# Kernel tuning notes

Measured on AMD Instinct MI355X. Metric: run time of the kernel, lower is better.

## Reference

```python
import jax, jax.numpy as jnp
import numpy as np

DIM = 1536
HEADS = 12
HEAD_DIM = DIM // HEADS
EPS = 1e-6
IMG_LEN = 257


def _rmsnorm(x, g):
    var = jnp.mean(jnp.square(x), axis=-1, keepdims=True)
    return x * jax.lax.rsqrt(var + EPS) * g


def _attn(q, k, v):
    # q: [b, Lq, h, d], k/v: [b, Lk, h, d]
    scale = 1.0 / jnp.sqrt(jnp.asarray(HEAD_DIM, q.dtype))
    s = jnp.einsum('bqhd,bkhd->bhqk', q, k) * scale
    p = jax.nn.softmax(s, axis=-1)
    return jnp.einsum('bhqk,bkhd->bqhd', p, v)


def setup_inputs() -> dict:
    key = jax.random.key(0)
    ks = jax.random.split(key, 20)
    w = lambda k: jax.random.normal(k, (DIM, DIM), dtype=jnp.float32) * 0.02
    b = lambda k: jax.random.normal(k, (DIM,), dtype=jnp.float32) * 0.01
    return {
        'x': jax.random.normal(ks[0], (1, 16384, DIM), dtype=jnp.float32),
        'context': jax.random.normal(ks[1], (1, 769, DIM), dtype=jnp.float32),
        'context_lens': jax.random.randint(ks[2], (1,), 0, 512, dtype=jnp.int32),
        'Wq': w(ks[3]), 'bq': b(ks[4]),
        'Wk': w(ks[5]), 'bk': b(ks[6]),
        'Wv': w(ks[7]), 'bv': b(ks[8]),
        'W_addk': w(ks[9]), 'b_addk': b(ks[10]),
        'W_addv': w(ks[11]), 'b_addv': b(ks[12]),
        'Wo': w(ks[13]), 'bo': b(ks[14]),
        'gq': jnp.ones((DIM,), dtype=jnp.float32),
        'gk': jnp.ones((DIM,), dtype=jnp.float32),
        'g_addk': jnp.ones((DIM,), dtype=jnp.float32),
    }


def reference(x, context, context_lens, Wq, bq, Wk, bk, Wv, bv,
              W_addk, b_addk, W_addv, b_addv, Wo, bo, gq, gk, g_addk):
    b_sz, L1, _ = x.shape
    ctx_img = context[:, :IMG_LEN]   # [B, 257, C]
    ctx_txt = context[:, IMG_LEN:]   # [B, L2-257, C]

    q = _rmsnorm(x @ Wq + bq, gq).reshape(b_sz, -1, HEADS, HEAD_DIM)
    k = _rmsnorm(ctx_txt @ Wk + bk, gk).reshape(b_sz, -1, HEADS, HEAD_DIM)
    v = (ctx_txt @ Wv + bv).reshape(b_sz, -1, HEADS, HEAD_DIM)
    k_img = _rmsnorm(ctx_img @ W_addk + b_addk, g_addk).reshape(b_sz, -1, HEADS, HEAD_DIM)
    v_img = (ctx_img @ W_addv + b_addv).reshape(b_sz, -1, HEADS, HEAD_DIM)

    img_x = _attn(q, k_img, v_img).reshape(b_sz, L1, DIM)
    txt_x = _attn(q, k, v).reshape(b_sz, L1, DIM)
    out = (txt_x + img_x) @ Wo + bo
    return out
```

## Files before the change

### kernel.cpp

```cpp
#include <hip/hip_runtime.h>
#include <cstdint>
#include <cstddef>

typedef unsigned short u16;
typedef unsigned int u32;
typedef short bfrag __attribute__((ext_vector_type(8)));
typedef __bf16 yfrag __attribute__((ext_vector_type(8)));
typedef float f4 __attribute__((ext_vector_type(4)));

__device__ __forceinline__ u16 f2bs(float f) {
  union { float f; u32 u; } x; x.f = f;
  u32 r = x.u + 0x7fffu + ((x.u >> 16) & 1u);
  return (u16)(r >> 16);
}
__device__ __forceinline__ float bs2f(u16 s) {
  union { u32 u; float f; } x; x.u = ((u32)s) << 16;
  return x.f;
}
__device__ __forceinline__ u32 cvtpk_bf16(float lo, float hi) {
  u32 d;
  asm("v_cvt_pk_bf16_f32 %0, %1, %2" : "=v"(d) : "v"(lo), "v"(hi));
  return d;
}

template <typename T>
__device__ __forceinline__ auto mfma_sel(T a, T b, f4 c, int)
    -> decltype(__builtin_amdgcn_mfma_f32_16x16x32_bf16(a, b, c, 0, 0, 0)) {
  return __builtin_amdgcn_mfma_f32_16x16x32_bf16(a, b, c, 0, 0, 0);
}
template <typename T>
__device__ __forceinline__ f4 mfma_sel(T a, T b, f4 c, long) {
  yfrag ya = __builtin_bit_cast(yfrag, a);
  yfrag yb = __builtin_bit_cast(yfrag, b);
  return __builtin_amdgcn_mfma_f32_16x16x32_bf16(ya, yb, c, 0, 0, 0);
}
__device__ __forceinline__ f4 MFMA(bfrag a, bfrag b, f4 c) {
  return mfma_sel(a, b, c, 0);
}

__device__ __forceinline__ void gl2lds16(const u16* g, u16* l) {
  __builtin_amdgcn_global_load_lds(
      (__attribute__((address_space(1))) void*)(g),
      (__attribute__((address_space(3))) void*)(l), 16, 0, 0);
}

__global__ __launch_bounds__(256) void cvt2(const float* __restrict__ x,
                                            u16* __restrict__ xbf,
                                            const float* __restrict__ ctx,
                                            u16* __restrict__ ctxb) {
  int i = blockIdx.x * 256 + threadIdx.x;
  const float* src; u16* dst;
  if (i < 3145728) {
    src = x; dst = xbf;
  } else {
    i -= 3145728;
    if (i >= 147648) return;
    src = ctx; dst = ctxb;
  }
  const float4* s4 = (const float4*)src;
  float4 a = s4[(size_t)i * 2];
  float4 b = s4[(size_t)i * 2 + 1];
  uint4 o;
  o.x = cvtpk_bf16(a.x, a.y);
  o.y = cvtpk_bf16(a.z, a.w);
  o.z = cvtpk_bf16(b.x, b.y);
  o.w = cvtpk_bf16(b.z, b.w);
  ((uint4*)dst)[i] = o;
}

__global__ __launch_bounds__(256) void transpose6(
    const float* s0, const float* s1, const float* s2, const float* s3,
    const float* s4, const float* s5, u16* d0, u16* d1, u16* d2, u16* d3,
    u16* d4, u16* d5) {
  const float* src; u16* dst;
  switch (blockIdx.z) {
    case 0: src = s0; dst = d0; break;
    case 1: src = s1; dst = d1; break;
    case 2: src = s2; dst = d2; break;
    case 3: src = s3; dst = d3; break;
    case 4: src = s4; dst = d4; break;
    default: src = s5; dst = d5; break;
  }
  __shared__ float tile[32][33];
  int tx = threadIdx.x, ty = threadIdx.y;
  int bx = blockIdx.x * 32, by = blockIdx.y * 32;
#pragma unroll
  for (int j = 0; j < 4; j++)
    tile[ty + j * 8][tx] = src[(size_t)(by + ty + j * 8) * 1536 + bx + tx];
  __syncthreads();
#pragma unroll
  for (int j = 0; j < 4; j++)
    dst[(size_t)(bx + ty + j * 8) * 1536 + by + tx] = f2bs(tile[tx][ty + j * 8]);
}

__device__ __forceinline__ void gemm_core(
    const u16* __restrict__ A, const u16* __restrict__ Bt,
    const float* __restrict__ bias, void* __restrict__ outp,
    int Mreal, int ldT, int epi, int bx, int by) {
  __shared__ u16 As[128 * 32];
  __shared__ u16 Bs[128 * 32];
  const int tid = threadIdx.x;
  const int w = tid >> 6, lane = tid & 63;
  const int quad = lane >> 4, l15 = lane & 15;
  const int m0 = bx * 128, n0 = by * 128;
  const int wm = (w >> 1) * 64, wn = (w & 1) * 64;

  f4 acc[4][4];
#pragma unroll
  for (int i = 0; i < 4; i++)
#pragma unroll
    for (int j = 0; j < 4; j++) acc[i][j] = f4{0.f, 0.f, 0.f, 0.f};

  const int c0 = w * 128 + lane;
  const int c1 = c0 + 64;
  const int ar0 = c0 >> 2, as0 = (c0 & 3) * 8;
  const int ar1 = c1 >> 2, as1 = (c1 & 3) * 8;
  const u16* Ab = A + (size_t)m0 * 1536;
  const u16* Bb = Bt + (size_t)n0 * 1536;
  u16* ldsA0 = As + (w * 2 + 0) * 512;
  u16* ldsA1 = As + (w * 2 + 1) * 512;
  u16* ldsB0 = Bs + (w * 2 + 0) * 512;
  u16* ldsB1 = Bs + (w * 2 + 1) * 512;

  for (int kt = 0; kt < 48; ++kt) {
    const int k0 = kt * 32;
    gl2lds16(Ab + (size_t)ar0 * 1536 + k0 + as0, ldsA0);
    gl2lds16(Ab + (size_t)ar1 * 1536 + k0 + as1, ldsA1);
    gl2lds16(Bb + (size_t)ar0 * 1536 + k0 + as0, ldsB0);
    gl2lds16(Bb + (size_t)ar1 * 1536 + k0 + as1, ldsB1);
    __syncthreads();
    bfrag af[4], bfr[4];
#pragma unroll
    for (int i = 0; i < 4; i++)
      af[i] = *(const bfrag*)(As + (wm + i * 16 + l15) * 32 + quad * 8);
#pragma unroll
    for (int j = 0; j < 4; j++)
      bfr[j] = *(const bfrag*)(Bs + (wn + j * 16 + l15) * 32 + quad * 8);
#pragma unroll
    for (int i = 0; i < 4; i++)
#pragma unroll
      for (int j = 0; j < 4; j++) acc[i][j] = MFMA(af[i], bfr[j], acc[i][j]);
    __syncthreads();
  }

  float bcol[4];
#pragma unroll
  for (int j = 0; j < 4; j++) bcol[j] = bias[n0 + wn + j * 16 + l15];

  if (epi == 1) {
    u16* dst = (u16*)outp;
#pragma unroll
    for (int i = 0; i < 4; i++)
#pragma unroll
      for (int r = 0; r < 4; r++) {
        int row = m0 + wm + i * 16 + quad * 4 + r;
        if (row < Mreal) {
#pragma unroll
          for (int j = 0; j < 4; j++) {
            int col = n0 + wn + j * 16 + l15;
            dst[(size_t)col * ldT + row] = f2bs(acc[i][j][r] + bcol[j]);
          }
        }
      }
  } else if (epi == 0) {
    u16* dst = (u16*)outp;
#pragma unroll
    for (int i = 0; i < 4; i++)
#pragma unroll
      for (int r = 0; r < 4; r++) {
        int row = m0 + wm + i * 16 + quad * 4 + r;
        if (row < Mreal) {
#pragma unroll
          for (int j = 0; j < 4; j++) {
            int col = n0 + wn + j * 16 + l15;
            dst[(size_t)row * 1536 + col] = f2bs(acc[i][j][r] + bcol[j]);
          }
        }
      }
  } else {
    float* dst = (float*)outp;
#pragma unroll
    for (int i = 0; i < 4; i++)
#pragma unroll
      for (int r = 0; r < 4; r++) {
        int row = m0 + wm + i * 16 + quad * 4 + r;
        if (row < Mreal) {
#pragma unroll
          for (int j = 0; j < 4; j++) {
            int col = n0 + wn + j * 16 + l15;
            dst[(size_t)row * 1536 + col] = acc[i][j][r] + bcol[j];
          }
        }
      }
  }
}

__global__ __launch_bounds__(256, 4) void gemm_bt(
    const u16* __restrict__ A, const u16* __restrict__ Bt,
    const float* __restrict__ bias, void* __restrict__ outp, int Mreal,
    int ldT, int epi) {
  gemm_core(A, Bt, bias, outp, Mreal, ldT, epi, blockIdx.x, blockIdx.y);
}

__global__ __launch_bounds__(256, 4) void gemm_multi(
    const u16* __restrict__ xbf, const u16* __restrict__ wqT,
    const float* __restrict__ bq, u16* __restrict__ qb,
    const u16* __restrict__ ctxb, const u16* __restrict__ wkT,
    const float* __restrict__ bk, u16* __restrict__ ktxt,
    const u16* __restrict__ wakT, const float* __restrict__ bak,
    u16* __restrict__ kimg, const u16* __restrict__ wvT,
    const float* __restrict__ bv, u16* __restrict__ vtt,
    const u16* __restrict__ wavT, const float* __restrict__ bav,
    u16* __restrict__ vti) {
  const int id = blockIdx.x;
  const u16* ctxt = ctxb + 257 * 1536;
  const u16* A; const u16* Bt; const float* bias; void* outp;
  int Mreal, ldT, epi, bx, by;
  if (id < 1536) {
    A = xbf; Bt = wqT; bias = bq; outp = qb;
    Mreal = 16384; ldT = 0; epi = 0; bx = id & 127; by = id >> 7;
  } else if (id < 1584) {
    int t = id - 1536;
    A = ctxt; Bt = wkT; bias = bk; outp = ktxt;
    Mreal = 512; ldT = 0; epi = 0; bx = t & 3; by = t >> 2;
  } else if (id < 1620) {
    int t = id - 1584;
    A = ctxb; Bt = wakT; bias = bak; outp = kimg;
    Mreal = 257; ldT = 0; epi = 0; bx = t % 3; by = t / 3;
  } else if (id < 1668) {
    int t = id - 1620;
    A = ctxt; Bt = wvT; bias = bv; outp = vtt;
    Mreal = 512; ldT = 512; epi = 1; bx = t & 3; by = t >> 2;
  } else {
    int t = id - 1668;
    A = ctxb; Bt = wavT; bias = bav; outp = vti;
    Mreal = 257; ldT = 264; epi = 1; bx = t % 3; by = t / 3;
  }
  gemm_core(A, Bt, bias, outp, Mreal, ldT, epi, bx, by);
}

__global__ __launch_bounds__(256) void rmsnorm_multi(
    u16* __restrict__ qb, const float* __restrict__ gq,
    u16* __restrict__ ktxt, const float* __restrict__ gk,
    u16* __restrict__ kimg, const float* __restrict__ gak) {
  int row = blockIdx.x;
  u16* buf; const float* g;
  if (row < 16384) {
    buf = qb; g = gq;
  } else if (row < 16896) {
    buf = ktxt; g = gk; row -= 16384;
  } else {
    buf = kimg; g = gak; row -= 16896;
  }
  const int tid = threadIdx.x;
  u16* p = buf + (size_t)row * 1536;
  float v[6];
  float ss = 0.f;
#pragma unroll
  for (int j = 0; j < 6; j++) {
    v[j] = bs2f(p[tid + j * 256]);
    ss += v[j] * v[j];
  }
#pragma unroll
  for (int off = 32; off; off >>= 1) ss += __shfl_xor(ss, off);
  __shared__ float red[4];
  if ((tid & 63) == 0) red[tid >> 6] = ss;
  __syncthreads();
  ss = red[0] + red[1] + red[2] + red[3];
  const float sc = rsqrtf(ss * (1.0f / 1536.0f) + 1e-6f);
#pragma unroll
  for (int j = 0; j < 6; j++)
    p[tid + j * 256] = f2bs(v[j] * sc * g[tid + j * 256]);
}

#define ATTN_SCALE 0.08838834764831845f
__global__ __launch_bounds__(256, 2) void attn_kernel(
    const u16* __restrict__ q, const u16* __restrict__ ktxt,
    const u16* __restrict__ kimg, const u16* __restrict__ vttxt,
    const u16* __restrict__ vtimg, u16* __restrict__ y) {
  __shared__ u16 Ks[64 * 128];
  __shared__ u16 Vs[128 * 64];
  __shared__ u16 Ps[4 * 32 * 72];
  const int tid = threadIdx.x;
  const int w = tid >> 6, lane = tid & 63;
  const int quad = lane >> 4, l15 = lane & 15;
  const int h = blockIdx.y, hoff = h * 128;
  const int mw = blockIdx.x * 128 + w * 32;
  u16* Pw = Ps + w * (32 * 72);

  bfrag qf[2][4];
#pragma unroll
  for (int rt = 0; rt < 2; rt++) {
    const u16* qrow = q + (size_t)(mw + rt * 16 + l15) * 1536 + hoff + quad * 8;
#pragma unroll
    for (int c = 0; c < 4; c++) qf[rt][c] = *(const bfrag*)(qrow + c * 32);
  }

  int kko[4], kco[4], vfe[4], vco[4];
#pragma unroll
  for (int j = 0; j < 4; j++) {
    int i = j * 256 + tid;
    int s = i >> 4, cp = i & 15;
    kko[j] = 4 * (s & 15) + (s >> 4);
    kco[j] = ((cp ^ (s & 7)) * 8);
    int f = i >> 3, cq = i & 7;
    vfe[j] = f;
    vco[j] = ((cq ^ (f & 7)) * 8);
  }

  f4 o[2][8];
  u32 resA[2][8][2];
  float lr[2][4];

  for (int seg = 0; seg < 2; seg++) {
    const u16* kp = seg ? ktxt : kimg;
    const u16* vp = seg ? vttxt : vtimg;
    const int Lk = seg ? 512 : 257;
    const int ldv = seg ? 512 : 264;
    const int nit = seg ? 8 : 5;
#pragma unroll
    for (int rt = 0; rt < 2; rt++) {
#pragma unroll
      for (int ft = 0; ft < 8; ft++) o[rt][ft] = f4{0.f, 0.f, 0.f, 0.f};
#pragma unroll
      for (int r = 0; r < 4; r++) lr[rt][r] = 0.f;
    }

    for (int it = 0; it < nit; ++it) {
      const int t0 = it * 64;
#pragma unroll
      for (int j = 0; j < 4; j++)
        gl2lds16(kp + (size_t)(t0 + kko[j]) * 1536 + hoff + kco[j],
                 Ks + (j * 256 + w * 64) * 8);
#pragma unroll
      for (int j = 0; j < 4; j++)
        gl2lds16(vp + (size_t)(hoff + vfe[j]) * ldv + t0 + vco[j],
                 Vs + (j * 256 + w * 64) * 8);
      __syncthreads();

      f4 s[2][4];
#pragma unroll
      for (int rt = 0; rt < 2; rt++)
#pragma unroll
        for (int t = 0; t < 4; t++) s[rt][t] = f4{0.f, 0.f, 0.f, 0.f};
#pragma unroll
      for (int t = 0; t < 4; t++) {
        const u16* kb = Ks + (t * 16 + l15) * 128;
        bfrag kf[4];
#pragma unroll
        for (int c = 0; c < 4; c++)
          kf[c] = *(const bfrag*)(kb + (((c * 4 + quad) ^ (l15 & 7)) * 8));
#pragma unroll
        for (int rt = 0; rt < 2; rt++)
#pragma unroll
          for (int c = 0; c < 4; c++)
            s[rt][t] = MFMA(qf[rt][c], kf[c], s[rt][t]);
      }

      if (t0 + 64 <= Lk) {
#pragma unroll
        for (int rt = 0; rt < 2; rt++)
#pragma unroll
          for (int t = 0; t < 4; t++)
#pragma unroll
            for (int r = 0; r < 4; r++) {
              float p = __expf(s[rt][t][r] * ATTN_SCALE);
              s[rt][t][r] = p;
              lr[rt][r] += p;
            }
      } else {
#pragma unroll
        for (int t = 0; t < 4; t++) {
          bool ok = (t0 + 4 * l15 + t) < Lk;
#pragma unroll
          for (int rt = 0; rt < 2; rt++)
#pragma unroll
            for (int r = 0; r < 4; r++) {
              float p = ok ? __expf(s[rt][t][r] * ATTN_SCALE) : 0.f;
              s[rt][t][r] = p;
              lr[rt][r] += p;
            }
        }
      }

#pragma unroll
      for (int rt = 0; rt < 2; rt++)
#pragma unroll
        for (int r = 0; r < 4; r++) {
          u32 lo = cvtpk_bf16(s[rt][0][r], s[rt][1][r]);
          u32 hi = cvtpk_bf16(s[rt][2][r], s[rt][3][r]);
          *(uint2*)(Pw + (rt * 16 + quad * 4 + r) * 72 + l15 * 4) =
              make_uint2(lo, hi);
        }
      asm volatile("s_waitcnt lgkmcnt(0)" ::: "memory");
      bfrag pf[2][2];
#pragma unroll
      for (int rt = 0; rt < 2; rt++)
#pragma unroll
        for (int hf = 0; hf < 2; hf++)
          pf[rt][hf] =
              *(const bfrag*)(Pw + (rt * 16 + l15) * 72 + hf * 32 + quad * 8);

#pragma unroll
      for (int ft = 0; ft < 8; ft++) {
        const u16* vb = Vs + (ft * 16 + l15) * 64;
#pragma unroll
        for (int hf = 0; hf < 2; hf++) {
          bfrag vf = *(const bfrag*)(vb + (((hf * 4 + quad) ^ (l15 & 7)) * 8));
#pragma unroll
          for (int rt = 0; rt < 2; rt++)
            o[rt][ft] = MFMA(pf[rt][hf], vf, o[rt][ft]);
        }
      }
      __syncthreads();
    }

#pragma unroll
    for (int rt = 0; rt < 2; rt++)
#pragma unroll
      for (int r = 0; r < 4; r++) {
        float v = lr[rt][r];
        v += __shfl_xor(v, 1);
        v += __shfl_xor(v, 2);
        v += __shfl_xor(v, 4);
        v += __shfl_xor(v, 8);
        lr[rt][r] = 1.0f / v;
      }
    if (seg == 0) {
#pragma unroll
      for (int rt = 0; rt < 2; rt++)
#pragma unroll
        for (int ft = 0; ft < 8; ft++) {
          resA[rt][ft][0] = cvtpk_bf16(o[rt][ft][0] * lr[rt][0],
                                       o[rt][ft][1] * lr[rt][1]);
          resA[rt][ft][1] = cvtpk_bf16(o[rt][ft][2] * lr[rt][2],
                                       o[rt][ft][3] * lr[rt][3]);
        }
    }
  }

#pragma unroll
  for (int rt = 0; rt < 2; rt++)
#pragma unroll
    for (int ft = 0; ft < 8; ft++) {
      float ra[4];
      ra[0] = bs2f((u16)(resA[rt][ft][0] & 0xffffu));
      ra[1] = bs2f((u16)(resA[rt][ft][0] >> 16));
      ra[2] = bs2f((u16)(resA[rt][ft][1] & 0xffffu));
      ra[3] = bs2f((u16)(resA[rt][ft][1] >> 16));
#pragma unroll
      for (int r = 0; r < 4; r++)
        y[(size_t)(mw + rt * 16 + quad * 4 + r) * 1536 + hoff + ft * 16 + l15] =
            f2bs(ra[r] + o[rt][ft][r] * lr[rt][r]);
    }
}

extern "C" void kernel_launch(void* const* d_in, const int* in_sizes, int n_in,
                              void* d_out, int out_size, void* d_ws,
                              size_t ws_size, hipStream_t stream) {
  const float* x   = (const float*)d_in[0];
  const float* ctx = (const float*)d_in[1];
  const float* Wq  = (const float*)d_in[3];
  const float* bq  = (const float*)d_in[4];
  const float* Wk  = (const float*)d_in[5];
  const float* bk  = (const float*)d_in[6];
  const float* Wv  = (const float*)d_in[7];
  const float* bv  = (const float*)d_in[8];
  const float* Wak = (const float*)d_in[9];
  const float* bak = (const float*)d_in[10];
  const float* Wav = (const float*)d_in[11];
  const float* bav = (const float*)d_in[12];
  const float* Wo  = (const float*)d_in[13];
  const float* bo  = (const float*)d_in[14];
  const float* gq  = (const float*)d_in[15];
  const float* gk  = (const float*)d_in[16];
  const float* gak = (const float*)d_in[17];
  float* out = (float*)d_out;

  u16* xbf  = (u16*)d_ws;
  u16* qb   = xbf + 25165824;
  u16* ctxb = qb + 25165824;
  u16* wqT  = ctxb + 1181184;
  u16* wkT  = wqT + 2359296;
  u16* wvT  = wkT + 2359296;
  u16* wakT = wvT + 2359296;
  u16* wavT = wakT + 2359296;
  u16* woT  = wavT + 2359296;
  u16* ktxt = woT + 2359296;
  u16* kimg = ktxt + 786432;
  u16* vti  = kimg + 394752;
  u16* vtt  = vti + 405504;

  cvt2<<<12865, 256, 0, stream>>>(x, xbf, ctx, ctxb);
  transpose6<<<dim3(48, 48, 6), dim3(32, 8), 0, stream>>>(
      Wq, Wk, Wv, Wak, Wav, Wo, wqT, wkT, wvT, wakT, wavT, woT);

  gemm_multi<<<1704, 256, 0, stream>>>(xbf, wqT, bq, qb,
                                       ctxb, wkT, bk, ktxt,
                                       wakT, bak, kimg,
                                       wvT, bv, vtt,
                                       wavT, bav, vti);

  rmsnorm_multi<<<17153, 256, 0, stream>>>(qb, gq, ktxt, gk, kimg, gak);

  attn_kernel<<<dim3(128, 12), 256, 0, stream>>>(qb, ktxt, kimg, vtt, vti, xbf);

  gemm_bt<<<dim3(128, 12), 256, 0, stream>>>(xbf, woT, bo, out, 16384, 0, 2);
}
```

Measured before the change: 568.2 us.

## Use 256x256 multi-stage pipelined GEMM with swizzled LDS and vectorize rmsnorm

Replaces the 128x128 single-buffered GEMM with a 512-thread 256x256 tile kernel. It uses a 4-stage global-to-LDS pipeline with explicit vmcnt waits, XOR-swizzled LDS layout, split A/B staging interleaved with MFMA, and s_setprio around the MFMA blocks. The same kernel now handles the projection batch and the output projection through a mode flag, using 128KB dynamic LDS. Rmsnorm is vectorized to 32-bit bf16 pair loads and packed conversions. The aim is to raise MFMA utilization and hide load latency, at the cost of fewer, larger blocks and some tail imbalance (e.g. 384 blocks for the output GEMM).

```diff
diff --git a/kernel.cpp b/kernel.cpp
--- a/kernel.cpp
+++ b/kernel.cpp
@@ -93,116 +93,153 @@
     dst[(size_t)(bx + ty + j * 8) * 1536 + by + tx] = f2bs(tile[tx][ty + j * 8]);
 }
 
-__device__ __forceinline__ void gemm_core(
+__device__ __forceinline__ void gemm256_core(
     const u16* __restrict__ A, const u16* __restrict__ Bt,
     const float* __restrict__ bias, void* __restrict__ outp,
-    int Mreal, int ldT, int epi, int bx, int by) {
-  __shared__ u16 As[128 * 32];
-  __shared__ u16 Bs[128 * 32];
+    int Mreal, int ldT, int epi, int bx, int by, u16* As, u16* Bs) {
   const int tid = threadIdx.x;
   const int w = tid >> 6, lane = tid & 63;
   const int quad = lane >> 4, l15 = lane & 15;
-  const int m0 = bx * 128, n0 = by * 128;
-  const int wm = (w >> 1) * 64, wn = (w & 1) * 64;
-
-  f4 acc[4][4];
-#pragma unroll
-  for (int i = 0; i < 4; i++)
+  const int wm = w >> 2, wn = w & 3;
+  const int m0 = bx * 256, n0 = by * 256;
+
+  f4 acc[8][4];
+#pragma unroll
+  for (int i = 0; i < 8; i++)
 #pragma unroll
     for (int j = 0; j < 4; j++) acc[i][j] = f4{0.f, 0.f, 0.f, 0.f};
 
-  const int c0 = w * 128 + lane;
-  const int c1 = c0 + 64;
-  const int ar0 = c0 >> 2, as0 = (c0 & 3) * 8;
-  const int ar1 = c1 >> 2, as1 = (c1 & 3) * 8;
+  const int r0 = tid >> 2;
+  const int c0s = ((tid & 3) ^ (r0 & 3)) * 8;
+  const int r1 = r0 + 128;
+  const int c1s = ((tid & 3) ^ (r1 & 3)) * 8;
   const u16* Ab = A + (size_t)m0 * 1536;
   const u16* Bb = Bt + (size_t)n0 * 1536;
-  u16* ldsA0 = As + (w * 2 + 0) * 512;
-  u16* ldsA1 = As + (w * 2 + 1) * 512;
-  u16* ldsB0 = Bs + (w * 2 + 0) * 512;
-  u16* ldsB1 = Bs + (w * 2 + 1) * 512;
+
+#define STAGE_A(t)                                                        \
+  {                                                                       \
+    const int s_ = (t) & 3, k_ = (t) * 32;                                \
+    gl2lds16(Ab + (size_t)r0 * 1536 + k_ + c0s, As + s_ * 8192 + w * 512);\
+    gl2lds16(Ab + (size_t)r1 * 1536 + k_ + c1s,                           \
+             As + s_ * 8192 + 4096 + w * 512);                            \
+  }
+#define STAGE_B(t)                                                        \
+  {                                                                       \
+    const int s_ = (t) & 3, k_ = (t) * 32;                                \
+    gl2lds16(Bb + (size_t)r0 * 1536 + k_ + c0s, Bs + s_ * 8192 + w * 512);\
+    gl2lds16(Bb + (size_t)r1 * 1536 + k_ + c1s,                           \
+             Bs + s_ * 8192 + 4096 + w * 512);                            \
+  }
+
+  STAGE_A(0); STAGE_B(0);
+  STAGE_A(1); STAGE_B(1);
+  STAGE_A(2); STAGE_B(2);
 
   for (int kt = 0; kt < 48; ++kt) {
-    const int k0 = kt * 32;
-    gl2lds16(Ab + (size_t)ar0 * 1536 + k0 + as0, ldsA0);
-    gl2lds16(Ab + (size_t)ar1 * 1536 + k0 + as1, ldsA1);
-    gl2lds16(Bb + (size_t)ar0 * 1536 + k0 + as0, ldsB0);
-    gl2lds16(Bb + (size_t)ar1 * 1536 + k0 + as1, ldsB1);
-    __syncthreads();
-    bfrag af[4], bfr[4];
-#pragma unroll
-    for (int i = 0; i < 4; i++)
-      af[i] = *(const bfrag*)(As + (wm + i * 16 + l15) * 32 + quad * 8);
-#pragma unroll
-    for (int j = 0; j < 4; j++)
-      bfr[j] = *(const bfrag*)(Bs + (wn + j * 16 + l15) * 32 + quad * 8);
-#pragma unroll
-    for (int i = 0; i < 4; i++)
-#pragma unroll
-      for (int j = 0; j < 4; j++) acc[i][j] = MFMA(af[i], bfr[j], acc[i][j]);
-    __syncthreads();
-  }
+    const int s = kt & 3;
+    const u16* Asb = As + s * 8192;
+    const u16* Bsb = Bs + s * 8192;
+    if (kt < 46)
+      asm volatile("s_waitcnt vmcnt(8)" ::: "memory");
+    else if (kt == 46)
+      asm volatile("s_waitcnt vmcnt(4)" ::: "memory");
+    else
+      asm volatile("s_waitcnt vmcnt(0)" ::: "memory");
+    asm volatile("s_waitcnt lgkmcnt(0)" ::: "memory");
+    asm volatile("s_barrier" ::: "memory");
+
+    bfrag af[8], bf[4];
+#pragma unroll
+    for (int nf = 0; nf < 4; nf++) {
+      const int rb = wn * 64 + nf * 16 + l15;
+      bf[nf] = *(const bfrag*)(Bsb + rb * 32 + ((quad ^ (rb & 3)) * 8));
+    }
+#pragma unroll
+    for (int mf = 0; mf < 4; mf++) {
+      const int r = wm * 128 + mf * 16 + l15;
+      af[mf] = *(const bfrag*)(Asb + r * 32 + ((quad ^ (r & 3)) * 8));
+    }
+    if (kt < 45) STAGE_A(kt + 3);
+    __builtin_amdgcn_s_setprio(1);
+#pragma unroll
+    for (int mf = 0; mf < 4; mf++)
+#pragma unroll
+      for (int nf = 0; nf < 4; nf++)
+        acc[mf][nf] = MFMA(af[mf], bf[nf], acc[mf][nf]);
+    __builtin_amdgcn_s_setprio(0);
+
+    asm volatile("s_waitcnt lgkmcnt(0)" ::: "memory");
+    asm volatile("s_barrier" ::: "memory");
+#pragma unroll
+    for (int mf = 4; mf < 8; mf++) {
+      const int r = wm * 128 + mf * 16 + l15;
+      af[mf] = *(const bfrag*)(Asb + r * 32 + ((quad ^ (r & 3)) * 8));
+    }
+    if (kt < 45) STAGE_B(kt + 3);
+    __builtin_amdgcn_s_setprio(1);
+#pragma unroll
+    for (int mf = 4; mf < 8; mf++)
+#pragma unroll
+      for (int nf = 0; nf < 4; nf++)
+        acc[mf][nf] = MFMA(af[mf], bf[nf], acc[mf][nf]);
+    __builtin_amdgcn_s_setprio(0);
+  }
+#undef STAGE_A
+#undef STAGE_B
 
   float bcol[4];
 #pragma unroll
-  for (int j = 0; j < 4; j++) bcol[j] = bias[n0 + wn + j * 16 + l15];
+  for (int nf = 0; nf < 4; nf++) bcol[nf] = bias[n0 + wn * 64 + nf * 16 + l15];
 
   if (epi == 1) {
     u16* dst = (u16*)outp;
 #pragma unroll
-    for (int i = 0; i < 4; i++)
+    for (int mf = 0; mf < 8; mf++)
 #pragma unroll
       for (int r = 0; r < 4; r++) {
-        int row = m0 + wm + i * 16 + quad * 4 + r;
+        int row = m0 + wm * 128 + mf * 16 + quad * 4 + r;
         if (row < Mreal) {
 #pragma unroll
-          for (int j = 0; j < 4; j++) {
-            int col = n0 + wn + j * 16 + l15;
-            dst[(size_t)col * ldT + row] = f2bs(acc[i][j][r] + bcol[j]);
+          for (int nf = 0; nf < 4; nf++) {
+            int col = n0 + wn * 64 + nf * 16 + l15;
+            dst[(size_t)col * ldT + row] = f2bs(acc[mf][nf][r] + bcol[nf]);
           }
         }
       }
   } else if (epi == 0) {
     u16* dst = (u16*)outp;
 #pragma unroll
-    for (int i = 0; i < 4; i++)
+    for (int mf = 0; mf < 8; mf++)
 #pragma unroll
       for (int r = 0; r < 4; r++) {
-        int row = m0 + wm + i * 16 + quad * 4 + r;
+        int row = m0 + wm * 128 + mf * 16 + quad * 4 + r;
         if (row < Mreal) {
 #pragma unroll
-          for (int j = 0; j < 4; j++) {
-            int col = n0 + wn + j * 16 + l15;
-            dst[(size_t)row * 1536 + col] = f2bs(acc[i][j][r] + bcol[j]);
+          for (int nf = 0; nf < 4; nf++) {
+            int col = n0 + wn * 64 + nf * 16 + l15;
+            dst[(size_t)row * 1536 + col] = f2bs(acc[mf][nf][r] + bcol[nf]);
           }
         }
       }
   } else {
     float* dst = (float*)outp;
 #pragma unroll
-    for (int i = 0; i < 4; i++)
+    for (int mf = 0; mf < 8; mf++)
 #pragma unroll
       for (int r = 0; r < 4; r++) {
-        int row = m0 + wm + i * 16 + quad * 4 + r;
+        int row = m0 + wm * 128 + mf * 16 + quad * 4 + r;
         if (row < Mreal) {
 #pragma unroll
-          for (int j = 0; j < 4; j++) {
-            int col = n0 + wn + j * 16 + l15;
-            dst[(size_t)row * 1536 + col] = acc[i][j][r] + bcol[j];
+          for (int nf = 0; nf < 4; nf++) {
+            int col = n0 + wn * 64 + nf * 16 + l15;
+            dst[(size_t)row * 1536 + col] = acc[mf][nf][r] + bcol[nf];
           }
         }
       }
   }
 }
 
-__global__ __launch_bounds__(256, 4) void gemm_bt(
-    const u16* __restrict__ A, const u16* __restrict__ Bt,
-    const float* __restrict__ bias, void* __restrict__ outp, int Mreal,
-    int ldT, int epi) {
-  gemm_core(A, Bt, bias, outp, Mreal, ldT, epi, blockIdx.x, blockIdx.y);
-}
-
-__global__ __launch_bounds__(256, 4) void gemm_multi(
+__global__ __launch_bounds__(512, 2) void gemm256(
     const u16* __restrict__ xbf, const u16* __restrict__ wqT,
     const float* __restrict__ bq, u16* __restrict__ qb,
     const u16* __restrict__ ctxb, const u16* __restrict__ wkT,
@@ -211,32 +248,40 @@
     u16* __restrict__ kimg, const u16* __restrict__ wvT,
     const float* __restrict__ bv, u16* __restrict__ vtt,
     const u16* __restrict__ wavT, const float* __restrict__ bav,
-    u16* __restrict__ vti) {
+    u16* __restrict__ vti, const u16* __restrict__ yb,
+    const u16* __restrict__ woT, const float* __restrict__ bo,
+    float* __restrict__ out, int mode) {
+  extern __shared__ u16 lds[];
+  u16* As = lds;
+  u16* Bs = lds + 32768;
   const int id = blockIdx.x;
   const u16* ctxt = ctxb + 257 * 1536;
   const u16* A; const u16* Bt; const float* bias; void* outp;
   int Mreal, ldT, epi, bx, by;
-  if (id < 1536) {
+  if (mode == 1) {
+    A = yb; Bt = woT; bias = bo; outp = out;
+    Mreal = 16384; ldT = 0; epi = 2; bx = id & 63; by = id >> 6;
+  } else if (id < 384) {
     A = xbf; Bt = wqT; bias = bq; outp = qb;
-    Mreal = 16384; ldT = 0; epi = 0; bx = id & 127; by = id >> 7;
-  } else if (id < 1584) {
-    int t = id - 1536;
+    Mreal = 16384; ldT = 0; epi = 0; bx = id & 63; by = id >> 6;
+  } else if (id < 396) {
+    int t = id - 384;
     A = ctxt; Bt = wkT; bias = bk; outp = ktxt;
-    Mreal = 512; ldT = 0; epi = 0; bx = t & 3; by = t >> 2;
-  } else if (id < 1620) {
-    int t = id - 1584;
+    Mreal = 512; ldT = 0; epi = 0; bx = t & 1; by = t >> 1;
+  } else if (id < 408) {
+    int t = id - 396;
     A = ctxb; Bt = wakT; bias = bak; outp = kimg;
-    Mreal = 257; ldT = 0; epi = 0; bx = t % 3; by = t / 3;
-  } else if (id < 1668) {
-    int t = id - 1620;
+    Mreal = 257; ldT = 0; epi = 0; bx = t & 1; by = t >> 1;
+  } else if (id < 420) {
+    int t = id - 408;
     A = ctxt; Bt = wvT; bias = bv; outp = vtt;
-    Mreal = 512; ldT = 512; epi = 1; bx = t & 3; by = t >> 2;
+    Mreal = 512; ldT = 512; epi = 1; bx = t & 1; by = t >> 1;
   } else {
-    int t = id - 1668;
+    int t = id - 420;
     A = ctxb; Bt = wavT; bias = bav; outp = vti;
-    Mreal = 257; ldT = 264; epi = 1; bx = t % 3; by = t / 3;
-  }
-  gemm_core(A, Bt, bias, outp, Mreal, ldT, epi, bx, by);
+    Mreal = 257; ldT = 264; epi = 1; bx = t & 1; by = t >> 1;
+  }
+  gemm256_core(A, Bt, bias, outp, Mreal, ldT, epi, bx, by, As, Bs);
 }
 
 __global__ __launch_bounds__(256) void rmsnorm_multi(
@@ -253,13 +298,17 @@
     buf = kimg; g = gak; row -= 16896;
   }
   const int tid = threadIdx.x;
-  u16* p = buf + (size_t)row * 1536;
+  u32* p = (u32*)(buf + (size_t)row * 1536);
+  const float2* g2 = (const float2*)g;
+  u32 d[3];
   float v[6];
   float ss = 0.f;
 #pragma unroll
-  for (int j = 0; j < 6; j++) {
-    v[j] = bs2f(p[tid + j * 256]);
-    ss += v[j] * v[j];
+  for (int j = 0; j < 3; j++) {
+    d[j] = p[tid + j * 256];
+    v[2 * j]     = bs2f((u16)(d[j] & 0xffffu));
+    v[2 * j + 1] = bs2f((u16)(d[j] >> 16));
+    ss += v[2 * j] * v[2 * j] + v[2 * j + 1] * v[2 * j + 1];
   }
 #pragma unroll
   for (int off = 32; off; off >>= 1) ss += __shfl_xor(ss, off);
@@ -269,8 +318,11 @@
   ss = red[0] + red[1] + red[2] + red[3];
   const float sc = rsqrtf(ss * (1.0f / 1536.0f) + 1e-6f);
 #pragma unroll
-  for (int j = 0; j < 6; j++)
-    p[tid + j * 256] = f2bs(v[j] * sc * g[tid + j * 256]);
+  for (int j = 0; j < 3; j++) {
+    float2 gg = g2[tid + j * 256];
+    p[tid + j * 256] =
+        cvtpk_bf16(v[2 * j] * sc * gg.x, v[2 * j + 1] * sc * gg.y);
+  }
 }
 
 #define ATTN_SCALE 0.08838834764831845f
@@ -495,15 +547,21 @@
   transpose6<<<dim3(48, 48, 6), dim3(32, 8), 0, stream>>>(
       Wq, Wk, Wv, Wak, Wav, Wo, wqT, wkT, wvT, wakT, wavT, woT);
 
-  gemm_multi<<<1704, 256, 0, stream>>>(xbf, wqT, bq, qb,
-                                       ctxb, wkT, bk, ktxt,
-                                       wakT, bak, kimg,
-                                       wvT, bv, vtt,
-                                       wavT, bav, vti);
+  gemm256<<<432, 512, 131072, stream>>>(xbf, wqT, bq, qb,
+                                        ctxb, wkT, bk, ktxt,
+                                        wakT, bak, kimg,
+                                        wvT, bv, vtt,
+                                        wavT, bav, vti,
+                                        xbf, woT, bo, out, 0);
 
   rmsnorm_multi<<<17153, 256, 0, stream>>>(qb, gq, ktxt, gk, kimg, gak);
 
   attn_kernel<<<dim3(128, 12), 256, 0, stream>>>(qb, ktxt, kimg, vtt, vti, xbf);
 
-  gemm_bt<<<dim3(128, 12), 256, 0, stream>>>(xbf, woT, bo, out, 16384, 0, 2);
-}
+  gemm256<<<384, 512, 131072, stream>>>(xbf, wqT, bq, qb,
+                                        ctxb, wkT, bk, ktxt,
+                                        wakT, bak, kimg,
+                                        wvT, bv, vtt,
+                                        wavT, bav, vti,
+                                        xbf, woT, bo, out, 1);
+}
```

Result: no change. 575.5 us (+1.3%).
